# Kernel optimization log

Hardware: AMD Instinct MI355X
Metric: run time of the kernel (lower is better)

Reference implementation:

```python
import jax, jax.numpy as jnp
import numpy as np

B, S, D, H = 2, 2048, 1024, 16
DH = D // H

def setup_inputs() -> dict:
    key = jax.random.key(0)
    k1, k2, k3, k4 = jax.random.split(key, 4)
    x = jax.random.normal(k1, (B, S, D), dtype=jnp.float32)
    # flax Dense kernels: [in_features, out_features]
    w_qkv = jax.random.normal(k2, (D, 3 * D), dtype=jnp.float32) / np.sqrt(D)
    w_out = jax.random.normal(k3, (D, D), dtype=jnp.float32) / np.sqrt(D)
    b_out = jax.random.normal(k4, (D,), dtype=jnp.float32) * 0.01
    return {"x": x, "w_qkv": w_qkv, "w_out": w_out, "b_out": b_out}

def reference(x, w_qkv, w_out, b_out):
    b, s, d = x.shape
    h, dh = H, d // H
    qkv = jnp.einsum('bsd,de->bse', x, w_qkv)           # [B,S,3D]
    qkv = qkv.reshape(b, s, 3, h, dh)
    qkv = jnp.transpose(qkv, (2, 0, 3, 1, 4))            # [3,B,H,S,DH]
    q, k, v = qkv[0], qkv[1], qkv[2]
    attn = jnp.einsum('bhqd,bhkd->bhqk', q, k) / jnp.sqrt(jnp.float32(dh))
    attn = jax.nn.softmax(attn, axis=-1)                 # [B,H,S,S]
    y = jnp.einsum('bhqk,bhkd->bhqd', attn, v)           # [B,H,S,DH]
    y = jnp.transpose(y, (0, 2, 1, 3)).reshape(b, s, d)  # [B,S,D]
    return jnp.einsum('bsd,de->bse', y, w_out) + b_out
```

## Files before the change

kernel.cpp:

```cpp
#include <hip/hip_runtime.h>
#include <stdint.h>

typedef __bf16 bf16_t;
typedef __bf16 bf16x8 __attribute__((ext_vector_type(8)));
typedef float f32x4 __attribute__((ext_vector_type(4)));
typedef float f32x16 __attribute__((ext_vector_type(16)));
typedef unsigned short u16;
typedef unsigned short u16x8 __attribute__((ext_vector_type(8)));
typedef unsigned int u32;
typedef unsigned int u32x4 __attribute__((ext_vector_type(4)));

#define DEVI __device__ __forceinline__


DEVI u16 bits(float f) { bf16_t h = (bf16_t)f; return __builtin_bit_cast(u16, h); }

DEVI void gld16(const void* g, void* l) {
  __builtin_amdgcn_global_load_lds(
      (const __attribute__((address_space(1))) unsigned int*)g,
      (__attribute__((address_space(3))) unsigned int*)l, 16, 0, 0);
}

DEVI bf16x8 ldsr(const u16* s, int row, int cg) {
  const int byte = row * 128 + ((cg ^ (row & 7)) << 4);
  return *(const bf16x8*)((const char*)s + byte);
}

DEVI bf16x8 ldsrV(const u16* s, int row, int cg) {
  const int byte = row * 256 + ((cg ^ (row & 15)) << 4);
  return *(const bf16x8*)((const char*)s + byte);
}

DEVI float exp2v(float x) { return __builtin_amdgcn_exp2f(x); }

DEVI u32 cvtpk(float lo, float hi) {
  u32 r;
  asm("v_cvt_pk_bf16_f32 %0, %1, %2" : "=v"(r) : "v"(lo), "v"(hi));
  return r;
}

#define MFMA16(a, b, c) __builtin_amdgcn_mfma_f32_16x16x32_bf16(a, b, c, 0, 0, 0)
#define MFMA32(a, b, c) __builtin_amdgcn_mfma_f32_32x32x16_bf16(a, b, c, 0, 0, 0)

#define MKFRAG(dst, S, B)                                              \
  {                                                                    \
    u32 a_ = cvtpk(S[(B) + 0], S[(B) + 1]);                            \
    u32 b_ = cvtpk(S[(B) + 4], S[(B) + 5]);                            \
    u32 c_ = cvtpk(S[(B) + 2], S[(B) + 3]);                            \
    u32 d_ = cvtpk(S[(B) + 6], S[(B) + 7]);                            \
    asm("v_permlane32_swap_b32 %0, %1" : "+v"(a_), "+v"(b_));          \
    asm("v_permlane32_swap_b32 %0, %1" : "+v"(c_), "+v"(d_));          \
    u32x4 u_ = {a_, c_, b_, d_};                                       \
    dst = __builtin_bit_cast(bf16x8, u_);                              \
  }

__global__ void __launch_bounds__(256) cvt8(const float* __restrict__ in,
                                            u16* __restrict__ out, int n8) {
  const int i = blockIdx.x * 256 + threadIdx.x;
  if (i >= n8) return;
  const f32x4* p = (const f32x4*)in;
  const f32x4 a = p[2 * i], b = p[2 * i + 1];
  u16x8 o;
#pragma unroll
  for (int j = 0; j < 4; ++j) { o[j] = bits(a[j]); o[4 + j] = bits(b[j]); }
  *(u16x8*)(out + (size_t)i * 8) = o;
}

__global__ void __launch_bounds__(256) tconv(const float* __restrict__ in,
                                             u16* __restrict__ out, int K, int N) {
  __shared__ float T[64][65];
  const int k0 = blockIdx.x * 64, n0 = blockIdx.y * 64;
  const int tid = threadIdx.x;
#pragma unroll
  for (int i = 0; i < 4; ++i) {
    const int c = i * 256 + tid;
    const int row = c >> 4, c4 = c & 15;
    const f32x4 v = *(const f32x4*)(in + (size_t)(k0 + row) * N + n0 + c4 * 4);
#pragma unroll
    for (int j = 0; j < 4; ++j) T[row][c4 * 4 + j] = v[j];
  }
  __syncthreads();
#pragma unroll
  for (int i = 0; i < 2; ++i) {
    const int c = i * 256 + tid;
    const int nrow = c >> 3, k8 = c & 7;
    u16x8 o;
#pragma unroll
    for (int j = 0; j < 8; ++j) o[j] = bits(T[k8 * 8 + j][nrow]);
    *(u16x8*)(out + (size_t)(n0 + nrow) * K + k0 + k8 * 8) = o;
  }
}

__global__ void __launch_bounds__(256) vtrans(const u16* __restrict__ Vrm,
                                              u16* __restrict__ Vt) {
  __shared__ u16 T[64][72];
  const int s0 = blockIdx.x * 64;
  const int bh = blockIdx.y;
  const int tid = threadIdx.x;
#pragma unroll
  for (int i = 0; i < 2; ++i) {
    const int c = i * 256 + tid, srow = c >> 3, c8 = c & 7;
    const u16x8 v = *(const u16x8*)(Vrm + ((size_t)bh * 2048 + s0 + srow) * 64 + c8 * 8);
#pragma unroll
    for (int j = 0; j < 8; ++j) T[srow][c8 * 8 + j] = v[j];
  }
  __syncthreads();
#pragma unroll
  for (int i = 0; i < 2; ++i) {
    const int c = i * 256 + tid, dr = c >> 3, s8 = c & 7;
    u16x8 o;
#pragma unroll
    for (int j = 0; j < 8; ++j) o[j] = T[s8 * 8 + j][dr];
    *(u16x8*)(Vt + ((size_t)bh * 64 + dr) * 2048 + s0 + s8 * 8) = o;
  }
}

template <int BN>
DEVI void gemm_core(const u16* __restrict__ A, const u16* __restrict__ Bt,
                    u16* As, u16* Bs, int m0, int n0, int Kdim,
                    f32x4 (&acc)[4][BN / 32]) {
  const int NF = BN / 32;
  const int tid = threadIdx.x;
  const int l = tid & 63, w = tid >> 6;
  const int lr = l & 15, lh = l >> 4;
  const int wr = w >> 1, wc = w & 1;
  for (int kt = 0; kt < Kdim; kt += 64) {
#pragma unroll
    for (int i = 0; i < 4; ++i) {
      const int cb = i * 256 + w * 64;
      const int c = cb + l;
      const int row = c >> 3;
      const int col = ((c & 7) ^ (row & 7)) << 3;
      gld16(A + (size_t)(m0 + row) * Kdim + kt + col, As + (size_t)cb * 8);
    }
#pragma unroll
    for (int i = 0; i < BN / 32; ++i) {
      const int cb = i * 256 + w * 64;
      const int c = cb + l;
      const int row = c >> 3;
      const int col = ((c & 7) ^ (row & 7)) << 3;
      gld16(Bt + (size_t)(n0 + row) * Kdim + kt + col, Bs + (size_t)cb * 8);
    }
    __syncthreads();
#pragma unroll
    for (int kk = 0; kk < 2; ++kk) {
      bf16x8 af[4], bfr[NF];
#pragma unroll
      for (int m = 0; m < 4; ++m) af[m] = ldsr(As, wr * 64 + m * 16 + lr, kk * 4 + lh);
#pragma unroll
      for (int n = 0; n < NF; ++n)
        bfr[n] = ldsr(Bs, wc * (BN / 2) + n * 16 + lr, kk * 4 + lh);
#pragma unroll
      for (int m = 0; m < 4; ++m)
#pragma unroll
        for (int n = 0; n < NF; ++n)
          acc[m][n] = MFMA16(af[m], bfr[n], acc[m][n]);
    }
    __syncthreads();
  }
}

__global__ void __launch_bounds__(256) gemm_qkv_k(const u16* __restrict__ A,
                                                  const u16* __restrict__ Bt,
                                                  u16* __restrict__ Qb,
                                                  u16* __restrict__ Kb,
                                                  u16* __restrict__ Vb) {
  __shared__ u16 As[128 * 64], Bs[128 * 64];
  const int m0 = blockIdx.y * 128, n0 = blockIdx.x * 128;
  f32x4 acc[4][4] = {};
  gemm_core<128>(A, Bt, As, Bs, m0, n0, 1024, acc);
  const int tid = threadIdx.x;
  const int l = tid & 63, w = tid >> 6;
  const int lr = l & 15, lh = l >> 4;
  const int wr = w >> 1, wc = w & 1;
#pragma unroll
  for (int n = 0; n < 4; ++n) {
    const int ng = n0 + wc * 64 + n * 16 + lr;
    const int sel = ng >> 10, h = (ng >> 6) & 15, dh = ng & 63;
    u16* dst = sel == 0 ? Qb : (sel == 1 ? Kb : Vb);
    const float qs = (sel == 0) ? 0.125f * 1.44269504f : 1.0f;
#pragma unroll
    for (int m = 0; m < 4; ++m) {
#pragma unroll
      for (int r = 0; r < 4; ++r) {
        const int mg = m0 + wr * 64 + m * 16 + lh * 4 + r;
        const int b = mg >> 11, s = mg & 2047;
        dst[((size_t)(b * 16 + h) * 2048 + s) * 64 + dh] = bits(acc[m][n][r] * qs);
      }
    }
  }
}

__global__ void __launch_bounds__(256) gemm_out_k(const u16* __restrict__ A,
                                                  const u16* __restrict__ Bt,
                                                  const float* __restrict__ bias,
                                                  float* __restrict__ out) {
  __shared__ u16 As[128 * 64], Bs[64 * 64];
  const int m0 = blockIdx.y * 128, n0 = blockIdx.x * 64;
  f32x4 acc[4][2] = {};
  gemm_core<64>(A, Bt, As, Bs, m0, n0, 1024, acc);
  const int tid = threadIdx.x;
  const int l = tid & 63, w = tid >> 6;
  const int lr = l & 15, lh = l >> 4;
  const int wr = w >> 1, wc = w & 1;
#pragma unroll
  for (int n = 0; n < 2; ++n) {
    const int ng = n0 + wc * 32 + n * 16 + lr;
    const float bv = bias[ng];
#pragma unroll
    for (int m = 0; m < 4; ++m) {
#pragma unroll
      for (int r = 0; r < 4; ++r) {
        const int mg = m0 + wr * 64 + m * 16 + lh * 4 + r;
        out[(size_t)mg * 1024 + ng] = acc[m][n][r] + bv;
      }
    }
  }
}

__global__ void __launch_bounds__(256) attn_k(const u16* __restrict__ Qb,
                                              const u16* __restrict__ Kb,
                                              const u16* __restrict__ Vt,
                                              u16* __restrict__ Yb) {
  __shared__ u16 Ks[2][128 * 64];
  __shared__ u16 Vs[2][64 * 128];
  const int tid = threadIdx.x;
  const int l = tid & 63, w = tid >> 6;
  const int lq = l & 31, hi = l >> 5;
  const int i0 = blockIdx.x;
  const int bid = (i0 & 7) * 64 + (i0 >> 3);
  const int bh = bid >> 4, qt = bid & 15;

  const u16* Qp = Qb + ((size_t)bh * 2048 + qt * 128 + w * 32 + lq) * 64;
  bf16x8 qf0 = *(const bf16x8*)(Qp + hi * 8);
  bf16x8 qf1 = *(const bf16x8*)(Qp + 16 + hi * 8);
  bf16x8 qf2 = *(const bf16x8*)(Qp + 32 + hi * 8);
  bf16x8 qf3 = *(const bf16x8*)(Qp + 48 + hi * 8);

  const u16* Kbase = Kb + (size_t)bh * 2048 * 64;
  const u16* Vbase = Vt + (size_t)bh * 64 * 2048;

  bf16x8 ones;
#pragma unroll
  for (int j = 0; j < 8; ++j) ones[j] = (bf16_t)1.0f;

  f32x16 acc0 = {}, acc1 = {};
  f32x16 accs = {};

#define STAGE(Ksb, Vsb, kv0)                                               \
  {                                                                        \
    _Pragma("unroll") for (int ii = 0; ii < 4; ++ii) {                     \
      const int cb = ii * 256 + w * 64;                                    \
      const int c = cb + l;                                                \
      const int krow = c >> 3;                                             \
      const int kcol = ((c & 7) ^ (krow & 7)) << 3;                        \
      gld16(Kbase + (size_t)((kv0) + krow) * 64 + kcol, (Ksb) + cb * 8);   \
      const int vrow = c >> 4;                                             \
      const int vcol = ((c & 15) ^ (vrow & 15)) << 3;                      \
      gld16(Vbase + (size_t)vrow * 2048 + (kv0) + vcol, (Vsb) + cb * 8);   \
    }                                                                      \
  }

  STAGE(Ks[0], Vs[0], 0);
  __syncthreads();
  int cur = 0;

  for (int t = 0; t < 16; ++t) {
    if (t + 1 < 16) STAGE(Ks[cur ^ 1], Vs[cur ^ 1], (t + 1) * 128);
    const u16* Ksc = Ks[cur];
    const u16* Vsc = Vs[cur];

#pragma unroll
    for (int h2 = 0; h2 < 2; ++h2) {
      f32x16 s0 = {}, s1 = {};
      __builtin_amdgcn_s_setprio(1);
#pragma unroll
      for (int ks = 0; ks < 4; ++ks) {
        const bf16x8 qk = ks == 0 ? qf0 : (ks == 1 ? qf1 : (ks == 2 ? qf2 : qf3));
        s0 = MFMA32(ldsr(Ksc, h2 * 64 + lq, ks * 2 + hi), qk, s0);
        s1 = MFMA32(ldsr(Ksc, h2 * 64 + 32 + lq, ks * 2 + hi), qk, s1);
      }
      __builtin_amdgcn_s_setprio(0);

#pragma unroll
      for (int i = 0; i < 16; ++i) { s0[i] = exp2v(s0[i]); s1[i] = exp2v(s1[i]); }

      bf16x8 pa0, pa1, pa2, pa3;
      MKFRAG(pa0, s0, 0);
      MKFRAG(pa1, s0, 8);
      MKFRAG(pa2, s1, 0);
      MKFRAG(pa3, s1, 8);
      __builtin_amdgcn_s_setprio(1);
      accs = MFMA32(pa0, ones, accs);
      acc0 = MFMA32(pa0, ldsrV(Vsc, lq, h2 * 8 + hi), acc0);
      acc1 = MFMA32(pa0, ldsrV(Vsc, 32 + lq, h2 * 8 + hi), acc1);
      accs = MFMA32(pa1, ones, accs);
      acc0 = MFMA32(pa1, ldsrV(Vsc, lq, h2 * 8 + 2 + hi), acc0);
      acc1 = MFMA32(pa1, ldsrV(Vsc, 32 + lq, h2 * 8 + 2 + hi), acc1);
      accs = MFMA32(pa2, ones, accs);
      acc0 = MFMA32(pa2, ldsrV(Vsc, lq, h2 * 8 + 4 + hi), acc0);
      acc1 = MFMA32(pa2, ldsrV(Vsc, 32 + lq, h2 * 8 + 4 + hi), acc1);
      accs = MFMA32(pa3, ones, accs);
      acc0 = MFMA32(pa3, ldsrV(Vsc, lq, h2 * 8 + 6 + hi), acc0);
      acc1 = MFMA32(pa3, ldsrV(Vsc, 32 + lq, h2 * 8 + 6 + hi), acc1);
      __builtin_amdgcn_s_setprio(0);
    }

    __syncthreads();
    cur ^= 1;
  }
#undef STAGE

  const int b = bh >> 4, h = bh & 15;
#pragma unroll
  for (int r = 0; r < 16; ++r) {
    const float sd = 1.0f / accs[r];
    const int row = (r & 3) + 8 * (r >> 2) + 4 * hi;
    const int sq = qt * 128 + w * 32 + row;
    u16* yp = Yb + ((size_t)b * 2048 + sq) * 1024 + h * 64;
    yp[lq] = bits(acc0[r] * sd);
    yp[32 + lq] = bits(acc1[r] * sd);
  }
}

extern "C" void kernel_launch(void* const* d_in, const int* in_sizes, int n_in,
                              void* d_out, int out_size, void* d_ws, size_t ws_size,
                              hipStream_t stream) {
  (void)in_sizes; (void)n_in; (void)out_size; (void)ws_size;
  const float* x     = (const float*)d_in[0];
  const float* w_qkv = (const float*)d_in[1];
  const float* w_out = (const float*)d_in[2];
  const float* b_out = (const float*)d_in[3];
  float* out = (float*)d_out;

  char* ws = (char*)d_ws;
  u16* xb    = (u16*)(ws);
  u16* wqkvT = (u16*)(ws + 8388608);
  u16* woutT = (u16*)(ws + 14680064);
  u16* Qb    = (u16*)(ws + 16777216);
  u16* Kb    = (u16*)(ws + 25165824);
  u16* Vrm   = (u16*)(ws + 33554432);
  u16* Vt    = (u16*)(ws + 41943040);
  u16* Yb    = xb;

  cvt8<<<2048, 256, 0, stream>>>(x, xb, 4194304 / 8);
  tconv<<<dim3(16, 48), 256, 0, stream>>>(w_qkv, wqkvT, 1024, 3072);
  tconv<<<dim3(16, 16), 256, 0, stream>>>(w_out, woutT, 1024, 1024);
  gemm_qkv_k<<<dim3(24, 32), 256, 0, stream>>>(xb, wqkvT, Qb, Kb, Vrm);
  vtrans<<<dim3(32, 32), 256, 0, stream>>>(Vrm, Vt);
  attn_k<<<512, 256, 0, stream>>>(Qb, Kb, Vt, Yb);
  gemm_out_k<<<dim3(16, 32), 256, 0, stream>>>(Yb, woutT, b_out, out);
}
```

Before: 124.7 us.

## Split attention KV tile across two wave groups with LDS reduction

The attention kernel now launches 512 threads per block. Each of the four query wave rows is duplicated into two wave groups, and each group processes one half of every 128-key tile instead of looping over both halves. At the end, the upper group writes its partial numerator and denominator accumulators to shared memory and the lower group adds them before normalizing. The aim is more waves per CU to hide latency, at the cost of an extra reduction through LDS, a barrier, and more register pressure under launch_bounds(512,4).

```diff
diff --git a/kernel.cpp b/kernel.cpp
--- a/kernel.cpp
+++ b/kernel.cpp
@@ -218,20 +218,26 @@
   }
 }
 
-__global__ void __launch_bounds__(256) attn_k(const u16* __restrict__ Qb,
-                                              const u16* __restrict__ Kb,
-                                              const u16* __restrict__ Vt,
-                                              u16* __restrict__ Yb) {
-  __shared__ u16 Ks[2][128 * 64];
-  __shared__ u16 Vs[2][64 * 128];
+__global__ void __launch_bounds__(512, 4) attn_k(const u16* __restrict__ Qb,
+                                                 const u16* __restrict__ Kb,
+                                                 const u16* __restrict__ Vt,
+                                                 u16* __restrict__ Yb) {
+  __shared__ char smem[65536];
+  u16* const KsA = (u16*)smem;
+  u16* const KsB = (u16*)(smem + 16384);
+  u16* const VsA = (u16*)(smem + 32768);
+  u16* const VsB = (u16*)(smem + 49152);
+
   const int tid = threadIdx.x;
   const int l = tid & 63, w = tid >> 6;
   const int lq = l & 31, hi = l >> 5;
+  const int qw = w & 3;
+  const int khalf = w >> 2;
   const int i0 = blockIdx.x;
   const int bid = (i0 & 7) * 64 + (i0 >> 3);
   const int bh = bid >> 4, qt = bid & 15;
 
-  const u16* Qp = Qb + ((size_t)bh * 2048 + qt * 128 + w * 32 + lq) * 64;
+  const u16* Qp = Qb + ((size_t)bh * 2048 + qt * 128 + qw * 32 + lq) * 64;
   bf16x8 qf0 = *(const bf16x8*)(Qp + hi * 8);
   bf16x8 qf1 = *(const bf16x8*)(Qp + 16 + hi * 8);
   bf16x8 qf2 = *(const bf16x8*)(Qp + 32 + hi * 8);
@@ -249,8 +255,8 @@
 
 #define STAGE(Ksb, Vsb, kv0)                                               \
   {                                                                        \
-    _Pragma("unroll") for (int ii = 0; ii < 4; ++ii) {                     \
-      const int cb = ii * 256 + w * 64;                                    \
+    _Pragma("unroll") for (int ii = 0; ii < 2; ++ii) {                     \
+      const int cb = ii * 512 + w * 64;                                    \
       const int c = cb + l;                                                \
       const int krow = c >> 3;                                             \
       const int kcol = ((c & 7) ^ (krow & 7)) << 3;                        \
@@ -261,62 +267,80 @@
     }                                                                      \
   }
 
-  STAGE(Ks[0], Vs[0], 0);
+  STAGE(KsA, VsA, 0);
   __syncthreads();
   int cur = 0;
 
   for (int t = 0; t < 16; ++t) {
-    if (t + 1 < 16) STAGE(Ks[cur ^ 1], Vs[cur ^ 1], (t + 1) * 128);
-    const u16* Ksc = Ks[cur];
-    const u16* Vsc = Vs[cur];
-
-#pragma unroll
-    for (int h2 = 0; h2 < 2; ++h2) {
-      f32x16 s0 = {}, s1 = {};
-      __builtin_amdgcn_s_setprio(1);
-#pragma unroll
-      for (int ks = 0; ks < 4; ++ks) {
-        const bf16x8 qk = ks == 0 ? qf0 : (ks == 1 ? qf1 : (ks == 2 ? qf2 : qf3));
-        s0 = MFMA32(ldsr(Ksc, h2 * 64 + lq, ks * 2 + hi), qk, s0);
-        s1 = MFMA32(ldsr(Ksc, h2 * 64 + 32 + lq, ks * 2 + hi), qk, s1);
-      }
-      __builtin_amdgcn_s_setprio(0);
-
-#pragma unroll
-      for (int i = 0; i < 16; ++i) { s0[i] = exp2v(s0[i]); s1[i] = exp2v(s1[i]); }
-
-      bf16x8 pa0, pa1, pa2, pa3;
-      MKFRAG(pa0, s0, 0);
-      MKFRAG(pa1, s0, 8);
-      MKFRAG(pa2, s1, 0);
-      MKFRAG(pa3, s1, 8);
-      __builtin_amdgcn_s_setprio(1);
-      accs = MFMA32(pa0, ones, accs);
-      acc0 = MFMA32(pa0, ldsrV(Vsc, lq, h2 * 8 + hi), acc0);
-      acc1 = MFMA32(pa0, ldsrV(Vsc, 32 + lq, h2 * 8 + hi), acc1);
-      accs = MFMA32(pa1, ones, accs);
-      acc0 = MFMA32(pa1, ldsrV(Vsc, lq, h2 * 8 + 2 + hi), acc0);
-      acc1 = MFMA32(pa1, ldsrV(Vsc, 32 + lq, h2 * 8 + 2 + hi), acc1);
-      accs = MFMA32(pa2, ones, accs);
-      acc0 = MFMA32(pa2, ldsrV(Vsc, lq, h2 * 8 + 4 + hi), acc0);
-      acc1 = MFMA32(pa2, ldsrV(Vsc, 32 + lq, h2 * 8 + 4 + hi), acc1);
-      accs = MFMA32(pa3, ones, accs);
-      acc0 = MFMA32(pa3, ldsrV(Vsc, lq, h2 * 8 + 6 + hi), acc0);
-      acc1 = MFMA32(pa3, ldsrV(Vsc, 32 + lq, h2 * 8 + 6 + hi), acc1);
-      __builtin_amdgcn_s_setprio(0);
-    }
+    u16* const Ksn = cur ? KsA : KsB;
+    u16* const Vsn = cur ? VsA : VsB;
+    if (t + 1 < 16) STAGE(Ksn, Vsn, (t + 1) * 128);
+    const u16* Ksc = cur ? KsB : KsA;
+    const u16* Vsc = cur ? VsB : VsA;
+
+    f32x16 s0 = {}, s1 = {};
+    __builtin_amdgcn_s_setprio(1);
+#pragma unroll
+    for (int ks = 0; ks < 4; ++ks) {
+      const bf16x8 qk = ks == 0 ? qf0 : (ks == 1 ? qf1 : (ks == 2 ? qf2 : qf3));
+      s0 = MFMA32(ldsr(Ksc, khalf * 64 + lq, ks * 2 + hi), qk, s0);
+      s1 = MFMA32(ldsr(Ksc, khalf * 64 + 32 + lq, ks * 2 + hi), qk, s1);
+    }
+    __builtin_amdgcn_s_setprio(0);
+
+#pragma unroll
+    for (int i = 0; i < 16; ++i) { s0[i] = exp2v(s0[i]); s1[i] = exp2v(s1[i]); }
+
+    bf16x8 pa0, pa1, pa2, pa3;
+    MKFRAG(pa0, s0, 0);
+    MKFRAG(pa1, s0, 8);
+    MKFRAG(pa2, s1, 0);
+    MKFRAG(pa3, s1, 8);
+    __builtin_amdgcn_s_setprio(1);
+    accs = MFMA32(pa0, ones, accs);
+    acc0 = MFMA32(pa0, ldsrV(Vsc, lq, khalf * 8 + hi), acc0);
+    acc1 = MFMA32(pa0, ldsrV(Vsc, 32 + lq, khalf * 8 + hi), acc1);
+    accs = MFMA32(pa1, ones, accs);
+    acc0 = MFMA32(pa1, ldsrV(Vsc, lq, khalf * 8 + 2 + hi), acc0);
+    acc1 = MFMA32(pa1, ldsrV(Vsc, 32 + lq, khalf * 8 + 2 + hi), acc1);
+    accs = MFMA32(pa2, ones, accs);
+    acc0 = MFMA32(pa2, ldsrV(Vsc, lq, khalf * 8 + 4 + hi), acc0);
+    acc1 = MFMA32(pa2, ldsrV(Vsc, 32 + lq, khalf * 8 + 4 + hi), acc1);
+    accs = MFMA32(pa3, ones, accs);
+    acc0 = MFMA32(pa3, ldsrV(Vsc, lq, khalf * 8 + 6 + hi), acc0);
+    acc1 = MFMA32(pa3, ldsrV(Vsc, 32 + lq, khalf * 8 + 6 + hi), acc1);
+    __builtin_amdgcn_s_setprio(0);
 
     __syncthreads();
     cur ^= 1;
   }
 #undef STAGE
+
+  float* const F = (float*)smem;
+  float* const Fp = F + (size_t)(tid & 255) * 49;
+  if (khalf) {
+#pragma unroll
+    for (int r = 0; r < 16; ++r) {
+      Fp[r] = acc0[r];
+      Fp[16 + r] = acc1[r];
+      Fp[32 + r] = accs[r];
+    }
+  }
+  __syncthreads();
+  if (khalf) return;
+#pragma unroll
+  for (int r = 0; r < 16; ++r) {
+    acc0[r] += Fp[r];
+    acc1[r] += Fp[16 + r];
+    accs[r] += Fp[32 + r];
+  }
 
   const int b = bh >> 4, h = bh & 15;
 #pragma unroll
   for (int r = 0; r < 16; ++r) {
     const float sd = 1.0f / accs[r];
     const int row = (r & 3) + 8 * (r >> 2) + 4 * hi;
-    const int sq = qt * 128 + w * 32 + row;
+    const int sq = qt * 128 + qw * 32 + row;
     u16* yp = Yb + ((size_t)b * 2048 + sq) * 1024 + h * 64;
     yp[lq] = bits(acc0[r] * sd);
     yp[32 + lq] = bits(acc1[r] * sd);
@@ -348,6 +372,6 @@
   tconv<<<dim3(16, 16), 256, 0, stream>>>(w_out, woutT, 1024, 1024);
   gemm_qkv_k<<<dim3(24, 32), 256, 0, stream>>>(xb, wqkvT, Qb, Kb, Vrm);
   vtrans<<<dim3(32, 32), 256, 0, stream>>>(Vrm, Vt);
-  attn_k<<<512, 256, 0, stream>>>(Qb, Kb, Vt, Yb);
+  attn_k<<<512, 512, 0, stream>>>(Qb, Kb, Vt, Yb);
   gemm_out_k<<<dim3(16, 32), 256, 0, stream>>>(Yb, woutT, b_out, out);
 }
```

After: 120.0 us. 3.8% less time.
